# Kernel tuning notes

Measured on AMD Instinct MI355X. Metric: run time of the kernel, lower is better.

## Reference

```python
import jax, jax.numpy as jnp
import numpy as np

N_VERTS = 262144
N_PAIRS = 8388608
DHAT = 0.05  # barrier activation distance
EPS = 1e-12


def setup_inputs() -> dict:
    key = jax.random.key(0)
    k1, k2, k3, k4, k5 = jax.random.split(key, 5)
    # rest positions in the unit square (2D collision mesh)
    rest_positions = jax.random.uniform(k1, (N_VERTS, 2), dtype=jnp.float32)
    # small displacement dof vector (flattened [N,2] field)
    Uu = jax.random.normal(k2, (N_VERTS * 2,), dtype=jnp.float32) * 1e-3
    # frozen broad-phase candidate vertex-edge pairs
    pair_v = jax.random.randint(k3, (N_PAIRS,), 0, N_VERTS)
    pair_e0 = jax.random.randint(k4, (N_PAIRS,), 0, N_VERTS)
    pair_e1 = jax.random.randint(k5, (N_PAIRS,), 0, N_VERTS)
    return {"Uu": Uu, "rest_positions": rest_positions,
            "pair_v": pair_v, "pair_e0": pair_e0, "pair_e1": pair_e1}


def reference(Uu, rest_positions, pair_v, pair_e0, pair_e1):
    # U = dof_manager.create_field(Uu): flat dofs -> [N, 2] displacement field
    coords = rest_positions + Uu.reshape(-1, 2)  # current coordinates [N, 2]

    # gather point-edge candidate geometry  (irregular access, memory-bound)
    p = coords[pair_v]    # [P, 2]
    a = coords[pair_e0]   # [P, 2]
    b = coords[pair_e1]   # [P, 2]

    # narrow phase: squared point-segment distance in 2D
    ab = b - a
    ap = p - a
    denom = jnp.sum(ab * ab, axis=-1)                      # [P]
    t = jnp.clip(jnp.sum(ap * ab, axis=-1) / jnp.maximum(denom, EPS), 0.0, 1.0)
    diff = ap - t[:, None] * ab
    d2 = jnp.sum(diff * diff, axis=-1)                     # squared distance [P]

    # IPC barrier on squared distances: b(d2) = -(d2 - dhat2)^2 * ln(d2/dhat2)
    dhat2 = jnp.float32(DHAT * DHAT)
    d2s = jnp.maximum(d2, EPS)  # safe log
    barrier = -(d2s - dhat2) ** 2 * jnp.log(d2s / dhat2)
    barrier_energy = jnp.sum(jnp.where(d2 < dhat2, barrier, 0.0))
    return barrier_energy
```

## Files before the change

### kernel.cpp

```cpp
#include <hip/hip_runtime.h>


constexpr int N_VERTS = 262144;
constexpr int N_PAIRS = 8388608;
constexpr float DHAT2 = 0.05f * 0.05f;
constexpr float INV_DHAT2 = 1.0f / DHAT2;
constexpr float EPSF = 1e-12f;

__global__ __launch_bounds__(256) void coords_k(const float4* __restrict__ Uu,
                                                const float4* __restrict__ rest,
                                                float4* __restrict__ coords) {
    int i = blockIdx.x * blockDim.x + threadIdx.x;
    float4 u = Uu[i];
    float4 r = rest[i];
    coords[i] = make_float4(u.x + r.x, u.y + r.y, u.z + r.z, u.w + r.w);
}

__global__ __launch_bounds__(256) void pairs_k(const float2* __restrict__ coords,
                                               const int4* __restrict__ pv,
                                               const int4* __restrict__ pe0,
                                               const int4* __restrict__ pe1,
                                               float* __restrict__ out) {
    float acc = 0.0f;
    const int nquads = N_PAIRS / 4;
    const int stride = gridDim.x * blockDim.x;

    for (int q = blockIdx.x * blockDim.x + threadIdx.x; q < nquads; q += stride) {
        int4 v4 = pv[q];
        int4 a4 = pe0[q];
        int4 b4 = pe1[q];
        int vi[4] = {v4.x, v4.y, v4.z, v4.w};
        int ai[4] = {a4.x, a4.y, a4.z, a4.w};
        int bi[4] = {b4.x, b4.y, b4.z, b4.w};

#pragma unroll
        for (int k = 0; k < 4; ++k) {
            float2 p = coords[vi[k]];
            float2 a = coords[ai[k]];
            float2 b = coords[bi[k]];

            float abx = b.x - a.x, aby = b.y - a.y;
            float apx = p.x - a.x, apy = p.y - a.y;

            float denom = fmaxf(abx * abx + aby * aby, EPSF);
            float t = (apx * abx + apy * aby) / denom;
            t = fminf(fmaxf(t, 0.0f), 1.0f);

            float dx = apx - t * abx;
            float dy = apy - t * aby;
            float d2 = dx * dx + dy * dy;

            float d2s = fmaxf(d2, EPSF);
            float dm = d2s - DHAT2;
            float term = -(dm * dm) * __logf(d2s * INV_DHAT2);
            acc += (d2 < DHAT2) ? term : 0.0f;
        }
    }

#pragma unroll
    for (int off = 32; off > 0; off >>= 1)
        acc += __shfl_down(acc, off, 64);

    __shared__ float wsum[4];
    int lane = threadIdx.x & 63;
    int wave = threadIdx.x >> 6;
    if (lane == 0) wsum[wave] = acc;
    __syncthreads();

    if (threadIdx.x == 0) {
        float s = wsum[0] + wsum[1] + wsum[2] + wsum[3];
        atomicAdd(out, s);
    }
}

extern "C" void kernel_launch(void* const* d_in, const int* in_sizes, int n_in,
                              void* d_out, int out_size, void* d_ws, size_t ws_size,
                              hipStream_t stream) {
    const float* Uu   = (const float*)d_in[0];
    const float* rest = (const float*)d_in[1];
    const int*   pv   = (const int*)d_in[2];
    const int*   pe0  = (const int*)d_in[3];
    const int*   pe1  = (const int*)d_in[4];
    float* out = (float*)d_out;

    float* coords = (float*)d_ws;

    {
        int nvec = (N_VERTS * 2) / 4;
        coords_k<<<nvec / 256, 256, 0, stream>>>(
            (const float4*)Uu, (const float4*)rest, (float4*)coords);
    }

    hipMemsetAsync(d_out, 0, sizeof(float) * out_size, stream);

    {
        int blocks = 2048;
        pairs_k<<<blocks, 256, 0, stream>>>(
            (const float2*)coords, (const int4*)pv, (const int4*)pe0,
            (const int4*)pe1, out);
    }
}
```

Before: 216.9 us.

## Process two index quads per iteration with nontemporal loads and fold memset

Each thread now handles two quads of pairs per loop iteration, issuing all 24 coordinate gathers before the arithmetic so more memory requests are in flight. Index streams are read with nontemporal loads so they do not pollute cache that the coords gathers need. The separate memset of the output is folded into the coords kernel, removing one launch. The cost is higher register pressure from the extra in-flight values.

```diff
diff --git a/kernel.cpp b/kernel.cpp
--- a/kernel.cpp
+++ b/kernel.cpp
@@ -7,53 +7,79 @@
 constexpr float INV_DHAT2 = 1.0f / DHAT2;
 constexpr float EPSF = 1e-12f;
 
+typedef int v4i __attribute__((ext_vector_type(4)));
+
 __global__ __launch_bounds__(256) void coords_k(const float4* __restrict__ Uu,
                                                 const float4* __restrict__ rest,
-                                                float4* __restrict__ coords) {
+                                                float4* __restrict__ coords,
+                                                float* __restrict__ out,
+                                                int out_n) {
     int i = blockIdx.x * blockDim.x + threadIdx.x;
     float4 u = Uu[i];
     float4 r = rest[i];
     coords[i] = make_float4(u.x + r.x, u.y + r.y, u.z + r.z, u.w + r.w);
+    if (blockIdx.x == 0 && threadIdx.x < (unsigned)out_n) out[threadIdx.x] = 0.0f;
 }
 
 __global__ __launch_bounds__(256) void pairs_k(const float2* __restrict__ coords,
-                                               const int4* __restrict__ pv,
-                                               const int4* __restrict__ pe0,
-                                               const int4* __restrict__ pe1,
+                                               const v4i* __restrict__ pv,
+                                               const v4i* __restrict__ pe0,
+                                               const v4i* __restrict__ pe1,
                                                float* __restrict__ out) {
     float acc = 0.0f;
     const int nquads = N_PAIRS / 4;
     const int stride = gridDim.x * blockDim.x;
+    const int tid = blockIdx.x * blockDim.x + threadIdx.x;
 
-    for (int q = blockIdx.x * blockDim.x + threadIdx.x; q < nquads; q += stride) {
-        int4 v4 = pv[q];
-        int4 a4 = pe0[q];
-        int4 b4 = pe1[q];
-        int vi[4] = {v4.x, v4.y, v4.z, v4.w};
-        int ai[4] = {a4.x, a4.y, a4.z, a4.w};
-        int bi[4] = {b4.x, b4.y, b4.z, b4.w};
+    for (int q0 = tid; q0 < nquads; q0 += 2 * stride) {
+        const int q1 = q0 + stride;
+        const bool two = (q1 < nquads);
+
+        v4i v0 = __builtin_nontemporal_load(pv + q0);
+        v4i a0 = __builtin_nontemporal_load(pe0 + q0);
+        v4i b0 = __builtin_nontemporal_load(pe1 + q0);
+        v4i v1 = {}, a1 = {}, b1 = {};
+        if (two) {
+            v1 = __builtin_nontemporal_load(pv + q1);
+            a1 = __builtin_nontemporal_load(pe0 + q1);
+            b1 = __builtin_nontemporal_load(pe1 + q1);
+        }
+
+        int vi[8] = {v0.x, v0.y, v0.z, v0.w, v1.x, v1.y, v1.z, v1.w};
+        int ai[8] = {a0.x, a0.y, a0.z, a0.w, a1.x, a1.y, a1.z, a1.w};
+        int bi[8] = {b0.x, b0.y, b0.z, b0.w, b1.x, b1.y, b1.z, b1.w};
+
+        const int np = two ? 8 : 4;
+
+        float2 P[8], A[8], B[8];
+#pragma unroll
+        for (int k = 0; k < 8; ++k) {
+            if (k < np) {
+                P[k] = coords[vi[k]];
+                A[k] = coords[ai[k]];
+                B[k] = coords[bi[k]];
+            }
+        }
 
 #pragma unroll
-        for (int k = 0; k < 4; ++k) {
-            float2 p = coords[vi[k]];
-            float2 a = coords[ai[k]];
-            float2 b = coords[bi[k]];
+        for (int k = 0; k < 8; ++k) {
+            if (k < np) {
+                float abx = B[k].x - A[k].x, aby = B[k].y - A[k].y;
+                float apx = P[k].x - A[k].x, apy = P[k].y - A[k].y;
 
-            float abx = b.x - a.x, aby = b.y - a.y;
-            float apx = p.x - a.x, apy = p.y - a.y;
+                float denom = fmaxf(abx * abx + aby * aby, EPSF);
+                float t = (apx * abx + apy * aby) / denom;
+                t = fminf(fmaxf(t, 0.0f), 1.0f);
 
-            float denom = fmaxf(abx * abx + aby * aby, EPSF);
-            float t = (apx * abx + apy * aby) / denom;
-            t = fminf(fmaxf(t, 0.0f), 1.0f);
+                float dx = apx - t * abx;
+                float dy = apy - t * aby;
+                float d2 = dx * dx + dy * dy;
 
-            float dx = apx - t * abx;
-            float dy = apy - t * aby;
-            float d2 = dx * dx + dy * dy;
-
-            float d2s = fmaxf(d2, EPSF);
-            float dm = d2s - DHAT2;
-            float term = -(dm * dm) * __logf(d2s * INV_DHAT2);
-            acc += (d2 < DHAT2) ? term : 0.0f;
+                float d2s = fmaxf(d2, EPSF);
+                float dm = d2s - DHAT2;
+                float term = -(dm * dm) * __logf(d2s * INV_DHAT2);
+                acc += (d2 < DHAT2) ? term : 0.0f;
+            }
         }
     }
 
@@ -88,15 +114,13 @@
     {
         int nvec = (N_VERTS * 2) / 4;
         coords_k<<<nvec / 256, 256, 0, stream>>>(
-            (const float4*)Uu, (const float4*)rest, (float4*)coords);
+            (const float4*)Uu, (const float4*)rest, (float4*)coords, out, out_size);
     }
-
-    hipMemsetAsync(d_out, 0, sizeof(float) * out_size, stream);
 
     {
         int blocks = 2048;
         pairs_k<<<blocks, 256, 0, stream>>>(
-            (const float2*)coords, (const int4*)pv, (const int4*)pe0,
-            (const int4*)pe1, out);
+            (const float2*)coords, (const v4i*)pv, (const v4i*)pe0,
+            (const v4i*)pe1, out);
     }
 }
```

Measured after the change: 225.6 us. 1.04x slower.
